# Optimization experiments

Measured on AMD Instinct MI355X. Metric: run time of the kernel, lower is better.

Reference implementation:

```python
import jax, jax.numpy as jnp
import numpy as np

B, N, F_IN, F_OUT, E = 8, 20000, 128, 128, 320000
ALPHA = 0.2  # LeakyReLU negative slope


def _xavier_normal(key, shape, gain=1.414):
    fan_in, fan_out = shape[0], shape[1]
    std = gain * np.sqrt(2.0 / (fan_in + fan_out))
    return jax.random.normal(key, shape, dtype=jnp.float32) * std


def setup_inputs() -> dict:
    key = jax.random.key(0)
    k1, k2, k3, k4, k5 = jax.random.split(key, 5)
    x = jax.random.normal(k1, (B, N, F_IN), dtype=jnp.float32)
    W = _xavier_normal(k2, (F_IN, F_OUT))
    a = _xavier_normal(k3, (2 * F_OUT, 1))
    # Edge list (src, dst). First N src are arange so every row has >=1 edge
    # (avoids div-by-zero in rowsum, matching a graph with no isolated sources).
    src_extra = jax.random.randint(k4, (E - N,), 0, N, dtype=jnp.int32)
    src = jnp.concatenate([jnp.arange(N, dtype=jnp.int32), src_extra])
    dst = jax.random.randint(k5, (E,), 0, N, dtype=jnp.int32)
    edge = jnp.stack([src, dst], axis=0)  # [2, E]
    return {"x": x, "W": W, "a": a, "edge": edge}


def reference(x, W, a, edge):
    # x: [B, N, F_in], W: [F_in, F_out], a: [2*F_out, 1], edge: [2, E]
    Fo = W.shape[1]
    n = x.shape[1]
    src, dst = edge[0], edge[1]
    h = jnp.einsum('bnf,fo->bno', x, W)  # [B, N, Fo]
    # cat(h[src], h[dst]) @ a  ==  (h @ a1)[src] + (h @ a2)[dst]
    a1, a2 = a[:Fo, 0], a[Fo:, 0]
    s = (h @ a1)[:, src] + (h @ a2)[:, dst]  # [B, E]
    score = jnp.where(s > 0, s, ALPHA * s)  # LeakyReLU
    e = jnp.exp(-score)  # [B, E]
    # spmm: h_prime[src] += e * h[dst]; rowsum[src] += e  (per batch)
    msg = e[..., None] * h[:, dst, :]  # [B, E, Fo]
    seg = jax.vmap(lambda m: jax.ops.segment_sum(m, src, num_segments=n))(msg)  # [B,N,Fo]
    rowsum = jax.vmap(lambda v: jax.ops.segment_sum(v, src, num_segments=n))(e)  # [B,N]
    h_prime = seg / rowsum[..., None]
    return jax.nn.elu(h_prime)  # concat=True -> ELU
```

## Files before the change

kernel.cpp:

```cpp
#include <hip/hip_runtime.h>

#define NB 8
#define NN 20000
#define FI 128
#define FO 128
#define NE 320000
#define ROWS (NB * NN)
#define LRALPHA 0.2f
#define ELLW 96

typedef short bf16x8 __attribute__((ext_vector_type(8)));
typedef float f32x4 __attribute__((ext_vector_type(4)));

static __device__ __forceinline__ float b2f(unsigned short u) {
  return __uint_as_float(((unsigned int)u) << 16);
}
static __device__ __forceinline__ unsigned short f2b(float f) {
  unsigned int u = __float_as_uint(f);
  return (unsigned short)((u + 0x7FFFu + ((u >> 16) & 1u)) >> 16);
}

__global__ __launch_bounds__(256) void wt_kernel(const float* __restrict__ W,
                                                 unsigned short* __restrict__ Wb,
                                                 int* __restrict__ cursor) {
  int idx = blockIdx.x * 256 + threadIdx.x;
  if (idx < FI * FO) {
    int k = idx >> 7, o = idx & 127;
    Wb[o * 128 + k] = f2b(W[idx]);
  }
  if (idx < NN) cursor[idx] = 0;
}

#define LDW 136

__global__ __launch_bounds__(256) void gemm_kernel(
    const float* __restrict__ x, const unsigned short* __restrict__ Wb,
    const float* __restrict__ a,
    unsigned short* __restrict__ hb,
    float* __restrict__ g1, float* __restrict__ g2) {
  __shared__ __align__(16) unsigned short Ws[128 * LDW];
  const int tid = threadIdx.x;

  {
    const bf16x8* wsrc = (const bf16x8*)Wb;
#pragma unroll
    for (int it = 0; it < 8; ++it) {
      int c = tid + it * 256;
      int o = c >> 4, seg = c & 15;
      *(bf16x8*)&Ws[o * LDW + seg * 8] = wsrc[c];
    }
  }

  const int wv = tid >> 6;
  const int lane = tid & 63;
  const int m = lane & 15;
  const int quad = lane >> 4;
  const size_t row0 = (size_t)blockIdx.x * 64 + wv * 16;

  const float* xr = x + (row0 + m) * 128;
  bf16x8 afr[4];
#pragma unroll
  for (int k0 = 0; k0 < 4; ++k0) {
    const float4* xp = (const float4*)(xr + k0 * 32 + quad * 8);
    float4 v0 = xp[0];
    float4 v1 = xp[1];
    union { bf16x8 v; unsigned short u[8]; } af;
    af.u[0] = f2b(v0.x); af.u[1] = f2b(v0.y);
    af.u[2] = f2b(v0.z); af.u[3] = f2b(v0.w);
    af.u[4] = f2b(v1.x); af.u[5] = f2b(v1.y);
    af.u[6] = f2b(v1.z); af.u[7] = f2b(v1.w);
    afr[k0] = af.v;
  }
  __syncthreads();

  f32x4 acc[8] = {};
#pragma unroll
  for (int k0 = 0; k0 < 4; ++k0) {
#pragma unroll
    for (int c = 0; c < 8; ++c) {
      bf16x8 bf = *(const bf16x8*)&Ws[(c * 16 + m) * LDW + k0 * 32 + quad * 8];
      acc[c] = __builtin_amdgcn_mfma_f32_16x16x32_bf16(afr[k0], bf, acc[c], 0, 0, 0);
    }
  }

  unsigned short* hp = hb + row0 * 128;
#pragma unroll
  for (int c = 0; c < 8; ++c)
#pragma unroll
    for (int r = 0; r < 4; ++r)
      hp[(quad * 4 + r) * 128 + c * 16 + m] = f2b(acc[c][r]);

  float a1v[8], a2v[8];
#pragma unroll
  for (int c = 0; c < 8; ++c) {
    a1v[c] = a[c * 16 + m];
    a2v[c] = a[128 + c * 16 + m];
  }
  float p1[4] = {}, p2[4] = {};
#pragma unroll
  for (int c = 0; c < 8; ++c)
#pragma unroll
    for (int r = 0; r < 4; ++r) {
      p1[r] = fmaf(acc[c][r], a1v[c], p1[r]);
      p2[r] = fmaf(acc[c][r], a2v[c], p2[r]);
    }
#pragma unroll
  for (int off = 1; off < 16; off <<= 1)
#pragma unroll
    for (int r = 0; r < 4; ++r) {
      p1[r] += __shfl_xor(p1[r], off, 64);
      p2[r] += __shfl_xor(p2[r], off, 64);
    }
  if (m == 0) {
    size_t rbase = row0 + quad * 4;
#pragma unroll
    for (int r = 0; r < 4; ++r) {
      g1[rbase + r] = p1[r];
      g2[rbase + r] = p2[r];
    }
  }
}

__global__ __launch_bounds__(256) void ell_scatter_kernel(
    const int* __restrict__ src, const int* __restrict__ dst,
    int* __restrict__ cursor, int* __restrict__ ell) {
  int e = blockIdx.x * 256 + threadIdx.x;
  if (e < NE) {
    int s = src[e];
    int d = dst[e];
    int slot = atomicAdd(&cursor[s], 1);
    if (slot < ELLW) ell[s * ELLW + slot] = d;
  }
}

__global__ __launch_bounds__(256) void gather_kernel(
    const unsigned short* __restrict__ hb, const float* __restrict__ g1,
    const float* __restrict__ g2, const int* __restrict__ degs,
    const int* __restrict__ ell, float* __restrict__ out) {
  const int bid = blockIdx.x;
  const int b = bid & 7;
  const int wv = threadIdx.x >> 6;
  const int i = (bid >> 3) * 4 + wv;
  const int lane = threadIdx.x & 63;
  const int deg = min(degs[i], ELLW);
  const int base = i * ELLW;
  const float g1i = g1[(size_t)b * NN + i];
  const float* g2b = g2 + (size_t)b * NN;
  const char* hrow = (const char*)(hb + (size_t)b * NN * 128) + lane * 4;

  float accLo = 0.f, accHi = 0.f;
  float rs = 0.f;
  for (int c0 = 0; c0 < deg; c0 += 64) {
    const int cnt = min(64, deg - c0);
    const int li = lane < cnt ? lane : cnt - 1;
    const int dvec = ell[base + c0 + li];
    float w = 0.f;
    if (lane < cnt) {
      float sv = g1i + g2b[dvec];
      float sc = fmaxf(sv, LRALPHA * sv);
      w = __expf(-sc);
    }
    rs += w;
    const int cr = (cnt + 3) & ~3;
    for (int j = 0; j < cr; j += 4) {
#pragma unroll
      for (int jj = 0; jj < 4; ++jj) {
        float wj = __shfl(w, j + jj, 64);
        int dj = __shfl(dvec, j + jj, 64);
        unsigned int u = *(const unsigned int*)(hrow + ((size_t)dj << 8));
        accLo = fmaf(wj, __uint_as_float(u << 16), accLo);
        accHi = fmaf(wj, __uint_as_float(u & 0xFFFF0000u), accHi);
      }
    }
  }
#pragma unroll
  for (int off = 1; off < 64; off <<= 1) rs += __shfl_xor(rs, off, 64);

  const float inv = 1.f / rs;
  float v0 = accLo * inv;
  float v1 = accHi * inv;
  float o0 = v0 > 0.f ? v0 : __expf(v0) - 1.f;
  float o1 = v1 > 0.f ? v1 : __expf(v1) - 1.f;
  float2* op = (float2*)(out + ((size_t)b * NN + i) * 128 + lane * 2);
  *op = make_float2(o0, o1);
}

extern "C" void kernel_launch(void* const* d_in, const int* in_sizes, int n_in,
                              void* d_out, int out_size, void* d_ws, size_t ws_size,
                              hipStream_t stream) {
  const float* x = (const float*)d_in[0];
  const float* W = (const float*)d_in[1];
  const float* a = (const float*)d_in[2];
  const int* edge = (const int*)d_in[3];
  const int* src = edge;
  const int* dst = edge + NE;
  float* out = (float*)d_out;

  char* p = (char*)d_ws;
  unsigned short* hb = (unsigned short*)p;  p += (size_t)ROWS * 128 * 2;
  float* g1 = (float*)p;                    p += (size_t)ROWS * 4;
  float* g2 = (float*)p;                    p += (size_t)ROWS * 4;
  int* cursor = (int*)p;                    p += (size_t)NN * 4;
  int* ell = (int*)p;                       p += (size_t)NN * ELLW * 4;
  unsigned short* Wb = (unsigned short*)p;  p += (size_t)FI * FO * 2;

  wt_kernel<<<80, 256, 0, stream>>>(W, Wb, cursor);
  gemm_kernel<<<ROWS / 64, 256, 0, stream>>>(x, Wb, a, hb, g1, g2);
  ell_scatter_kernel<<<(NE + 255) / 256, 256, 0, stream>>>(src, dst, cursor, ell);
  gather_kernel<<<(NN / 4) * NB, 256, 0, stream>>>(hb, g1, g2, cursor, ell, out);
}
```

Baseline: 260.1 us.

## Fuse scatter, GEMM and gather into one persistent kernel with grid barrier

Replaces the separate ELL scatter, GEMM and gather launches with a single persistent kernel of 1024 blocks. Each block does grid-strided scatter and GEMM tiles, then meets the others at a global atomic spin barrier before the gather phase. The goal is to remove launch gaps and kernel-boundary drains, and to overlap the atomic scatter with GEMM work. The cost is a software grid barrier that can deadlock if not all 1024 blocks are co-resident. The persistent loop also spreads gather work less evenly than the one-row-per-wave launch it replaces.

```diff
diff --git a/kernel.cpp b/kernel.cpp
--- a/kernel.cpp
+++ b/kernel.cpp
@@ -8,6 +8,9 @@
 #define ROWS (NB * NN)
 #define LRALPHA 0.2f
 #define ELLW 96
+#define NBLK 1024
+#define NTHR 256
+#define LDW 136
 
 typedef short bf16x8 __attribute__((ext_vector_type(8)));
 typedef float f32x4 __attribute__((ext_vector_type(4)));
@@ -20,26 +23,38 @@
   return (unsigned short)((u + 0x7FFFu + ((u >> 16) & 1u)) >> 16);
 }
 
-__global__ __launch_bounds__(256) void wt_kernel(const float* __restrict__ W,
-                                                 unsigned short* __restrict__ Wb,
-                                                 int* __restrict__ cursor) {
+__global__ __launch_bounds__(256) void init_kernel(const float* __restrict__ W,
+                                                   unsigned short* __restrict__ Wb,
+                                                   int* __restrict__ cursor,
+                                                   unsigned int* __restrict__ bar) {
   int idx = blockIdx.x * 256 + threadIdx.x;
   if (idx < FI * FO) {
     int k = idx >> 7, o = idx & 127;
     Wb[o * 128 + k] = f2b(W[idx]);
   }
   if (idx < NN) cursor[idx] = 0;
-}
-
-#define LDW 136
-
-__global__ __launch_bounds__(256) void gemm_kernel(
+  if (idx < 8) bar[idx] = 0;
+}
+
+__global__ __launch_bounds__(NTHR, 4) void mega_kernel(
     const float* __restrict__ x, const unsigned short* __restrict__ Wb,
-    const float* __restrict__ a,
-    unsigned short* __restrict__ hb,
-    float* __restrict__ g1, float* __restrict__ g2) {
+    const float* __restrict__ a, const int* __restrict__ src,
+    const int* __restrict__ dst, unsigned short* __restrict__ hb,
+    float* __restrict__ g1, float* __restrict__ g2, int* __restrict__ cursor,
+    int* __restrict__ ell, unsigned int* __restrict__ bar,
+    float* __restrict__ out) {
   __shared__ __align__(16) unsigned short Ws[128 * LDW];
   const int tid = threadIdx.x;
+  const int bid = blockIdx.x;
+  const int wv = tid >> 6;
+  const int lane = tid & 63;
+
+  for (int e = bid * NTHR + tid; e < NE; e += NBLK * NTHR) {
+    int s = src[e];
+    int d = dst[e];
+    int slot = atomicAdd(&cursor[s], 1);
+    if (slot < ELLW) ell[s * ELLW + slot] = d;
+  }
 
   {
     const bf16x8* wsrc = (const bf16x8*)Wb;
@@ -49,140 +64,124 @@
       int o = c >> 4, seg = c & 15;
       *(bf16x8*)&Ws[o * LDW + seg * 8] = wsrc[c];
     }
-  }
-
-  const int wv = tid >> 6;
-  const int lane = tid & 63;
-  const int m = lane & 15;
-  const int quad = lane >> 4;
-  const size_t row0 = (size_t)blockIdx.x * 64 + wv * 16;
-
-  const float* xr = x + (row0 + m) * 128;
-  bf16x8 afr[4];
-#pragma unroll
-  for (int k0 = 0; k0 < 4; ++k0) {
-    const float4* xp = (const float4*)(xr + k0 * 32 + quad * 8);
-    float4 v0 = xp[0];
-    float4 v1 = xp[1];
-    union { bf16x8 v; unsigned short u[8]; } af;
-    af.u[0] = f2b(v0.x); af.u[1] = f2b(v0.y);
-    af.u[2] = f2b(v0.z); af.u[3] = f2b(v0.w);
-    af.u[4] = f2b(v1.x); af.u[5] = f2b(v1.y);
-    af.u[6] = f2b(v1.z); af.u[7] = f2b(v1.w);
-    afr[k0] = af.v;
-  }
+    __syncthreads();
+    const int m = lane & 15;
+    const int quad = lane >> 4;
+    float a1v[8], a2v[8];
+#pragma unroll
+    for (int c = 0; c < 8; ++c) {
+      a1v[c] = a[c * 16 + m];
+      a2v[c] = a[128 + c * 16 + m];
+    }
+    for (int t = bid; t < ROWS / 64; t += NBLK) {
+      const size_t row0 = (size_t)t * 64 + wv * 16;
+      const float* xr = x + (row0 + m) * 128;
+      bf16x8 afr[4];
+#pragma unroll
+      for (int k0 = 0; k0 < 4; ++k0) {
+        const float4* xp = (const float4*)(xr + k0 * 32 + quad * 8);
+        float4 v0 = xp[0], v1 = xp[1];
+        union { bf16x8 v; unsigned short u[8]; } af;
+        af.u[0] = f2b(v0.x); af.u[1] = f2b(v0.y);
+        af.u[2] = f2b(v0.z); af.u[3] = f2b(v0.w);
+        af.u[4] = f2b(v1.x); af.u[5] = f2b(v1.y);
+        af.u[6] = f2b(v1.z); af.u[7] = f2b(v1.w);
+        afr[k0] = af.v;
+      }
+      f32x4 acc[8] = {};
+#pragma unroll
+      for (int k0 = 0; k0 < 4; ++k0)
+#pragma unroll
+        for (int c = 0; c < 8; ++c) {
+          bf16x8 bf = *(const bf16x8*)&Ws[(c * 16 + m) * LDW + k0 * 32 + quad * 8];
+          acc[c] = __builtin_amdgcn_mfma_f32_16x16x32_bf16(afr[k0], bf, acc[c], 0, 0, 0);
+        }
+      unsigned short* hp = hb + row0 * 128;
+#pragma unroll
+      for (int c = 0; c < 8; ++c)
+#pragma unroll
+        for (int r = 0; r < 4; ++r)
+          hp[(quad * 4 + r) * 128 + c * 16 + m] = f2b(acc[c][r]);
+      float p1[4] = {}, p2[4] = {};
+#pragma unroll
+      for (int c = 0; c < 8; ++c)
+#pragma unroll
+        for (int r = 0; r < 4; ++r) {
+          p1[r] = fmaf(acc[c][r], a1v[c], p1[r]);
+          p2[r] = fmaf(acc[c][r], a2v[c], p2[r]);
+        }
+#pragma unroll
+      for (int off = 1; off < 16; off <<= 1)
+#pragma unroll
+        for (int r = 0; r < 4; ++r) {
+          p1[r] += __shfl_xor(p1[r], off, 64);
+          p2[r] += __shfl_xor(p2[r], off, 64);
+        }
+      if (m == 0) {
+        size_t rbase = row0 + quad * 4;
+#pragma unroll
+        for (int r = 0; r < 4; ++r) {
+          g1[rbase + r] = p1[r];
+          g2[rbase + r] = p2[r];
+        }
+      }
+    }
+  }
+
   __syncthreads();
-
-  f32x4 acc[8] = {};
-#pragma unroll
-  for (int k0 = 0; k0 < 4; ++k0) {
-#pragma unroll
-    for (int c = 0; c < 8; ++c) {
-      bf16x8 bf = *(const bf16x8*)&Ws[(c * 16 + m) * LDW + k0 * 32 + quad * 8];
-      acc[c] = __builtin_amdgcn_mfma_f32_16x16x32_bf16(afr[k0], bf, acc[c], 0, 0, 0);
-    }
-  }
-
-  unsigned short* hp = hb + row0 * 128;
-#pragma unroll
-  for (int c = 0; c < 8; ++c)
-#pragma unroll
-    for (int r = 0; r < 4; ++r)
-      hp[(quad * 4 + r) * 128 + c * 16 + m] = f2b(acc[c][r]);
-
-  float a1v[8], a2v[8];
-#pragma unroll
-  for (int c = 0; c < 8; ++c) {
-    a1v[c] = a[c * 16 + m];
-    a2v[c] = a[128 + c * 16 + m];
-  }
-  float p1[4] = {}, p2[4] = {};
-#pragma unroll
-  for (int c = 0; c < 8; ++c)
-#pragma unroll
-    for (int r = 0; r < 4; ++r) {
-      p1[r] = fmaf(acc[c][r], a1v[c], p1[r]);
-      p2[r] = fmaf(acc[c][r], a2v[c], p2[r]);
-    }
-#pragma unroll
-  for (int off = 1; off < 16; off <<= 1)
-#pragma unroll
-    for (int r = 0; r < 4; ++r) {
-      p1[r] += __shfl_xor(p1[r], off, 64);
-      p2[r] += __shfl_xor(p2[r], off, 64);
-    }
-  if (m == 0) {
-    size_t rbase = row0 + quad * 4;
-#pragma unroll
-    for (int r = 0; r < 4; ++r) {
-      g1[rbase + r] = p1[r];
-      g2[rbase + r] = p2[r];
-    }
-  }
-}
-
-__global__ __launch_bounds__(256) void ell_scatter_kernel(
-    const int* __restrict__ src, const int* __restrict__ dst,
-    int* __restrict__ cursor, int* __restrict__ ell) {
-  int e = blockIdx.x * 256 + threadIdx.x;
-  if (e < NE) {
-    int s = src[e];
-    int d = dst[e];
-    int slot = atomicAdd(&cursor[s], 1);
-    if (slot < ELLW) ell[s * ELLW + slot] = d;
-  }
-}
-
-__global__ __launch_bounds__(256) void gather_kernel(
-    const unsigned short* __restrict__ hb, const float* __restrict__ g1,
-    const float* __restrict__ g2, const int* __restrict__ degs,
-    const int* __restrict__ ell, float* __restrict__ out) {
-  const int bid = blockIdx.x;
-  const int b = bid & 7;
-  const int wv = threadIdx.x >> 6;
-  const int i = (bid >> 3) * 4 + wv;
-  const int lane = threadIdx.x & 63;
-  const int deg = min(degs[i], ELLW);
-  const int base = i * ELLW;
-  const float g1i = g1[(size_t)b * NN + i];
-  const float* g2b = g2 + (size_t)b * NN;
-  const char* hrow = (const char*)(hb + (size_t)b * NN * 128) + lane * 4;
-
-  float accLo = 0.f, accHi = 0.f;
-  float rs = 0.f;
-  for (int c0 = 0; c0 < deg; c0 += 64) {
-    const int cnt = min(64, deg - c0);
-    const int li = lane < cnt ? lane : cnt - 1;
-    const int dvec = ell[base + c0 + li];
-    float w = 0.f;
-    if (lane < cnt) {
-      float sv = g1i + g2b[dvec];
-      float sc = fmaxf(sv, LRALPHA * sv);
-      w = __expf(-sc);
-    }
-    rs += w;
-    const int cr = (cnt + 3) & ~3;
-    for (int j = 0; j < cr; j += 4) {
-#pragma unroll
-      for (int jj = 0; jj < 4; ++jj) {
-        float wj = __shfl(w, j + jj, 64);
-        int dj = __shfl(dvec, j + jj, 64);
-        unsigned int u = *(const unsigned int*)(hrow + ((size_t)dj << 8));
-        accLo = fmaf(wj, __uint_as_float(u << 16), accLo);
-        accHi = fmaf(wj, __uint_as_float(u & 0xFFFF0000u), accHi);
+  if (tid == 0) {
+    __threadfence();
+    atomicAdd(&bar[0], 1u);
+    while (atomicAdd(&bar[0], 0u) < NBLK) __builtin_amdgcn_s_sleep(4);
+    __threadfence();
+  }
+  __syncthreads();
+
+  {
+    const int b = bid & 7;
+    const float* g1b = g1 + (size_t)b * NN;
+    const float* g2b = g2 + (size_t)b * NN;
+    const char* hrow = (const char*)(hb + (size_t)b * NN * 128) + lane * 4;
+    for (int i = (bid >> 3) * 4 + wv; i < NN; i += (NBLK / 8) * 4) {
+      const int deg = min(cursor[i], ELLW);
+      const int base = i * ELLW;
+      const float g1i = g1b[i];
+      float accLo = 0.f, accHi = 0.f;
+      float rs = 0.f;
+      for (int c0 = 0; c0 < deg; c0 += 64) {
+        const int cnt = min(64, deg - c0);
+        const int li = lane < cnt ? lane : cnt - 1;
+        const int dvec = ell[base + c0 + li];
+        float w = 0.f;
+        if (lane < cnt) {
+          float sv = g1i + g2b[dvec];
+          float sc = fmaxf(sv, LRALPHA * sv);
+          w = __expf(-sc);
+        }
+        rs += w;
+        const int cr = (cnt + 3) & ~3;
+        for (int j = 0; j < cr; j += 4) {
+#pragma unroll
+          for (int jj = 0; jj < 4; ++jj) {
+            float wj = __shfl(w, j + jj, 64);
+            int dj = __shfl(dvec, j + jj, 64);
+            unsigned int u = *(const unsigned int*)(hrow + ((size_t)dj << 8));
+            accLo = fmaf(wj, __uint_as_float(u << 16), accLo);
+            accHi = fmaf(wj, __uint_as_float(u & 0xFFFF0000u), accHi);
+          }
+        }
       }
-    }
-  }
-#pragma unroll
-  for (int off = 1; off < 64; off <<= 1) rs += __shfl_xor(rs, off, 64);
-
-  const float inv = 1.f / rs;
-  float v0 = accLo * inv;
-  float v1 = accHi * inv;
-  float o0 = v0 > 0.f ? v0 : __expf(v0) - 1.f;
-  float o1 = v1 > 0.f ? v1 : __expf(v1) - 1.f;
-  float2* op = (float2*)(out + ((size_t)b * NN + i) * 128 + lane * 2);
-  *op = make_float2(o0, o1);
+#pragma unroll
+      for (int off = 1; off < 64; off <<= 1) rs += __shfl_xor(rs, off, 64);
+      const float inv = 1.f / rs;
+      float v0 = accLo * inv;
+      float v1 = accHi * inv;
+      float o0 = v0 > 0.f ? v0 : __expf(v0) - 1.f;
+      float o1 = v1 > 0.f ? v1 : __expf(v1) - 1.f;
+      float2* op = (float2*)(out + ((size_t)b * NN + i) * 128 + lane * 2);
+      *op = make_float2(o0, o1);
+    }
+  }
 }
 
 extern "C" void kernel_launch(void* const* d_in, const int* in_sizes, int n_in,
@@ -203,9 +202,9 @@
   int* cursor = (int*)p;                    p += (size_t)NN * 4;
   int* ell = (int*)p;                       p += (size_t)NN * ELLW * 4;
   unsigned short* Wb = (unsigned short*)p;  p += (size_t)FI * FO * 2;
-
-  wt_kernel<<<80, 256, 0, stream>>>(W, Wb, cursor);
-  gemm_kernel<<<ROWS / 64, 256, 0, stream>>>(x, Wb, a, hb, g1, g2);
-  ell_scatter_kernel<<<(NE + 255) / 256, 256, 0, stream>>>(src, dst, cursor, ell);
-  gather_kernel<<<(NN / 4) * NB, 256, 0, stream>>>(hb, g1, g2, cursor, ell, out);
-}
+  unsigned int* bar = (unsigned int*)p;     p += 8 * 4;
+
+  init_kernel<<<80, 256, 0, stream>>>(W, Wb, cursor, bar);
+  mega_kernel<<<NBLK, NTHR, 0, stream>>>(x, Wb, a, src, dst, hb, g1, g2,
+                                         cursor, ell, bar, out);
+}
```

Result: slower. 518.3 us (+99.3%).
